# Performance work log

Hardware: AMD Instinct MI355X
Metric: run time of the kernel (lower is better)

The kernel has to match this reference:

```python
import jax, jax.numpy as jnp
import numpy as np

L, B, E, H, V, T = 512, 64, 256, 256, 32000, 50


def setup_inputs() -> dict:
    key = jax.random.key(0)
    ks = jax.random.split(key, 8)
    s_cell = 1.0 / np.sqrt(H + E)
    s_out = 1.0 / np.sqrt(2 * H)
    return {
        "text": jax.random.randint(ks[0], (L, B), 0, V, dtype=jnp.int64),
        "emb": jax.random.normal(ks[1], (V, E), dtype=jnp.float32),
        "W_f": jax.random.uniform(ks[2], (H, H + E), jnp.float32, -s_cell, s_cell),
        "b_f": jax.random.uniform(ks[3], (H,), jnp.float32, -s_cell, s_cell),
        "W_b": jax.random.uniform(ks[4], (H, H + E), jnp.float32, -s_cell, s_cell),
        "b_b": jax.random.uniform(ks[5], (H,), jnp.float32, -s_cell, s_cell),
        "W_out": jax.random.uniform(ks[6], (T, 2 * H), jnp.float32, -s_out, s_out),
        "b_out": jax.random.uniform(ks[7], (T,), jnp.float32, -s_out, s_out),
    }


def _rnn_scan(x_seq, W, b, batch, hidden):
    # x_seq: [L, B, E]; cell: h' = sigmoid(Linear(cat([x, h])))
    h0 = jnp.zeros((batch, hidden), dtype=x_seq.dtype)

    def step(h, x):
        h_new = jax.nn.sigmoid(jnp.concatenate([x, h], axis=1) @ W.T + b)
        return h_new, h_new

    _, hs = jax.lax.scan(step, h0, x_seq)
    return hs  # [L, B, H]


def reference(text, emb, W_f, b_f, W_b, b_b, W_out, b_out):
    # text: [L, B] int
    x = emb[text]  # [L, B, E]
    lr = _rnn_scan(x, W_f, b_f, x.shape[1], W_f.shape[0])  # [L, B, H]
    # backward cell processes reversed input; rl_tensor[i] = hidden after
    # processing positions L-1 .. L-1-i (NOT re-flipped, matching the source).
    rl = _rnn_scan(x[::-1], W_b, b_b, x.shape[1], W_b.shape[0])  # [L, B, H]
    hidden = jnp.concatenate([lr, rl], axis=2)  # [L, B, 2H]
    out = hidden @ W_out.T + b_out  # [L, B, T]
    return out, hidden
```

## Files before the change

kernel.cpp:

```cpp
#include <hip/hip_runtime.h>
#include <stdint.h>

#define L_SEQ 512
#define BATCH 64
#define KTOT  512
#define TDIM  50
#define HID2  512
#define ROWSTRIDE ((long)BATCH * HID2)
#define NLOG2E 1.4426950408889634f

typedef __attribute__((ext_vector_type(8))) short bf16x8;
typedef __attribute__((ext_vector_type(4))) float f32x4;

static __device__ __forceinline__ unsigned short f2bf(float f) {
  union { float f; unsigned int u; } v; v.f = f;
  unsigned int r = (v.u + 0x7FFFu + ((v.u >> 16) & 1u)) >> 16;
  return (unsigned short)r;
}

static __device__ __forceinline__ bf16x8 pack8(const float* f) {
  bf16x8 r;
#pragma unroll
  for (int i = 0; i < 8; ++i) r[i] = (short)f2bf(f[i]);
  return r;
}

static __device__ __forceinline__ unsigned cvt_pk_bf16(float a, float b) {
  unsigned r;
  asm("v_cvt_pk_bf16_f32 %0, %1, %2" : "=v"(r) : "v"(a), "v"(b));
  return r;
}

__global__ __launch_bounds__(512) void pre_kernel(
    const int* __restrict__ text, const float* __restrict__ emb,
    const float* __restrict__ W_f, const float* __restrict__ b_f,
    const float* __restrict__ W_b, const float* __restrict__ b_b,
    float* __restrict__ hidden) {
  const int blk = blockIdx.x;
  const int dir = blk >> 8;
  const int base = (blk & 255) * 128;
  const float* W    = dir ? W_b : W_f;
  const float* bias = dir ? b_b : b_f;
  const int tid = threadIdx.x;
  const int w = tid >> 6, ln = tid & 63, m16 = ln & 15, g4 = ln >> 4;

  __shared__ __align__(16) unsigned char xLds[16 * 512];

  bf16x8 wfrag[2][8];
#pragma unroll
  for (int t = 0; t < 2; ++t) {
    const int j0 = w * 32 + t * 16 + m16;
#pragma unroll
    for (int kk = 0; kk < 8; ++kk) {
      const float* p = W + (long)j0 * KTOT + kk * 32 + g4 * 8;
      float4 p0 = *(const float4*)(p);
      float4 p1 = *(const float4*)(p + 4);
      float f[8] = {p0.x, p0.y, p0.z, p0.w, p1.x, p1.y, p1.z, p1.w};
      wfrag[t][kk] = pack8(f);
    }
  }
  float biasr[2][4];
#pragma unroll
  for (int t = 0; t < 2; ++t)
#pragma unroll
    for (int r = 0; r < 4; ++r) biasr[t][r] = bias[w * 32 + t * 16 + 4 * g4 + r];

  const int xm = tid >> 5;
  const int e0 = (tid & 31) * 8;

  for (int mt = 0; mt < 8; ++mt) {
    const int g = base + mt * 16 + xm;
    const int l = g >> 6, b = g & 63;
    const int srcl = dir ? (L_SEQ - 1 - l) : l;
    const int tok = text[srcl * BATCH + b];
    const float* xp = emb + (long)tok * 256 + e0;
    float4 a0 = *(const float4*)(xp);
    float4 a1 = *(const float4*)(xp + 4);
    float f[8] = {a0.x, a0.y, a0.z, a0.w, a1.x, a1.y, a1.z, a1.w};
    bf16x8 xv = pack8(f);
    if (mt) __syncthreads();
    *(bf16x8*)(xLds + xm * 512 + ((e0 * 2) ^ ((xm & 7) << 4))) = xv;
    __syncthreads();

    f32x4 acc0 = {0.f, 0.f, 0.f, 0.f};
    f32x4 acc1 = {0.f, 0.f, 0.f, 0.f};
#pragma unroll
    for (int kk = 0; kk < 8; ++kk) {
      bf16x8 uf = *(const bf16x8*)(xLds + m16 * 512 +
                                   (((kk * 64) + g4 * 16) ^ ((m16 & 7) << 4)));
      acc0 = __builtin_amdgcn_mfma_f32_16x16x32_bf16(wfrag[0][kk], uf, acc0, 0, 0, 0);
      acc1 = __builtin_amdgcn_mfma_f32_16x16x32_bf16(wfrag[1][kk], uf, acc1, 0, 0, 0);
    }
    const int gg = base + mt * 16 + m16;
    float* op = hidden + (long)gg * HID2 + dir * 256 + w * 32 + 4 * g4;
    *(float4*)(op)      = make_float4(-NLOG2E * (acc0[0] + biasr[0][0]),
                                      -NLOG2E * (acc0[1] + biasr[0][1]),
                                      -NLOG2E * (acc0[2] + biasr[0][2]),
                                      -NLOG2E * (acc0[3] + biasr[0][3]));
    *(float4*)(op + 16) = make_float4(-NLOG2E * (acc1[0] + biasr[1][0]),
                                      -NLOG2E * (acc1[1] + biasr[1][1]),
                                      -NLOG2E * (acc1[2] + biasr[1][2]),
                                      -NLOG2E * (acc1[3] + biasr[1][3]));
  }
}

__global__ __launch_bounds__(512, 1) void scan_kernel(
    const float* __restrict__ W_f, const float* __restrict__ W_b,
    float* __restrict__ hidden) {
  const int wg  = blockIdx.x;
  const int dir = wg >> 2;
  const int b0  = (wg & 3) * 16;
  const int tid = threadIdx.x;
  const int w = tid >> 6, ln = tid & 63, m16 = ln & 15, g4 = ln >> 4;
  const float* W = dir ? W_b : W_f;

  __shared__ __align__(16) unsigned char hLds[2][8 * 1024];

  bf16x8 wfrag[2][8];
#pragma unroll
  for (int t = 0; t < 2; ++t) {
    const int j0 = w * 32 + t * 16 + m16;
#pragma unroll
    for (int kk = 0; kk < 8; ++kk) {
      const float* p = W + (long)j0 * KTOT + 256 + kk * 32 + g4 * 8;
      float4 p0 = *(const float4*)(p);
      float4 p1 = *(const float4*)(p + 4);
      float f[8] = {-NLOG2E * p0.x, -NLOG2E * p0.y, -NLOG2E * p0.z, -NLOG2E * p0.w,
                    -NLOG2E * p1.x, -NLOG2E * p1.y, -NLOG2E * p1.z, -NLOG2E * p1.w};
      wfrag[t][kk] = pack8(f);
    }
  }

  int rdoff[8];
#pragma unroll
  for (int kk = 0; kk < 8; ++kk) rdoff[kk] = kk * 1024 + ln * 16;
  const int wroff0 = w * 1024 + ((g4 >> 1) * 256) + m16 * 16 + (g4 & 1) * 8;
  const int wroff1 = wroff0 + 512;

  *(f32x4*)(&hLds[0][0] + tid * 16) = f32x4{0.f, 0.f, 0.f, 0.f};

  const long roff = (long)(b0 + m16) * HID2 + dir * 256 + w * 32 + 4 * g4;

  f32x4 pA0, pA1, pB0, pB1;
  pA0 = *(const f32x4*)(hidden + roff);
  pA1 = *(const f32x4*)(hidden + roff + 16);
  pB0 = *(const f32x4*)(hidden + ROWSTRIDE + roff);
  pB1 = *(const f32x4*)(hidden + ROWSTRIDE + roff + 16);

  __syncthreads();

#define STEP(BUF, PF0, PF1, SROW)                                              \
  {                                                                            \
    bf16x8 uf[8];                                                              \
    _Pragma("unroll")                                                          \
    for (int kk = 0; kk < 8; ++kk)                                             \
      uf[kk] = *(const bf16x8*)(&hLds[BUF][0] + rdoff[kk]);                    \
    f32x4 acc0 = {0.f, 0.f, 0.f, 0.f};                                         \
    f32x4 acc1 = {0.f, 0.f, 0.f, 0.f};                                         \
    _Pragma("unroll")                                                          \
    for (int kk = 0; kk < 8; ++kk) {                                           \
      acc0 = __builtin_amdgcn_mfma_f32_16x16x32_bf16(wfrag[0][kk], uf[kk],     \
                                                     acc0, 0, 0, 0);           \
      acc1 = __builtin_amdgcn_mfma_f32_16x16x32_bf16(wfrag[1][kk], uf[kk],     \
                                                     acc1, 0, 0, 0);           \
    }                                                                          \
    float h0[4], h1[4];                                                        \
    _Pragma("unroll")                                                          \
    for (int r = 0; r < 4; ++r) {                                              \
      h0[r] = __builtin_amdgcn_rcpf(                                           \
          1.f + __builtin_amdgcn_exp2f(acc0[r] + PF0[r]));                     \
      h1[r] = __builtin_amdgcn_rcpf(                                           \
          1.f + __builtin_amdgcn_exp2f(acc1[r] + PF1[r]));                     \
    }                                                                          \
    *(uint2*)(&hLds[(BUF) ^ 1][0] + wroff0) =                                  \
        make_uint2(cvt_pk_bf16(h0[0], h0[1]), cvt_pk_bf16(h0[2], h0[3]));      \
    *(uint2*)(&hLds[(BUF) ^ 1][0] + wroff1) =                                  \
        make_uint2(cvt_pk_bf16(h1[0], h1[1]), cvt_pk_bf16(h1[2], h1[3]));      \
    float* gp = hidden + (long)(SROW)*ROWSTRIDE + roff;                        \
    *(float4*)(gp)      = make_float4(h0[0], h0[1], h0[2], h0[3]);             \
    *(float4*)(gp + 16) = make_float4(h1[0], h1[1], h1[2], h1[3]);             \
    {                                                                          \
      const long rn = ((SROW) + 2 < L_SEQ) ? (SROW) + 2 : L_SEQ - 1;           \
      const float* lp = hidden + rn * ROWSTRIDE + roff;                        \
      PF0 = *(const f32x4*)(lp);                                               \
      PF1 = *(const f32x4*)(lp + 16);                                          \
    }                                                                          \
    asm volatile("s_waitcnt lgkmcnt(0)" ::: "memory");                         \
    __builtin_amdgcn_s_barrier();                                              \
    asm volatile("" ::: "memory");                                             \
  }

  for (int s = 0; s < L_SEQ; s += 2) {
    STEP(0, pA0, pA1, s)
    STEP(1, pB0, pB1, s + 1)
  }
#undef STEP
}

__global__ __launch_bounds__(64) void out_kernel(
    const float* __restrict__ hidden, const float* __restrict__ W_out,
    const float* __restrict__ b_out, float* __restrict__ out) {
  const int m0 = blockIdx.x * 16;
  const int ln = threadIdx.x;
  const int m16 = ln & 15, g4 = ln >> 4;

  bf16x8 a[16];
  const float* hp = hidden + (long)(m0 + m16) * HID2 + g4 * 8;
#pragma unroll
  for (int kk = 0; kk < 16; ++kk) {
    float4 p0 = *(const float4*)(hp + kk * 32);
    float4 p1 = *(const float4*)(hp + kk * 32 + 4);
    float f[8] = {p0.x, p0.y, p0.z, p0.w, p1.x, p1.y, p1.z, p1.w};
    a[kk] = pack8(f);
  }
#pragma unroll
  for (int nt = 0; nt < 4; ++nt) {
    const int trow = nt * 16 + m16;
    const bool valid = trow < TDIM;
    f32x4 acc = {0.f, 0.f, 0.f, 0.f};
    const float* wp = W_out + (long)trow * HID2 + g4 * 8;
#pragma unroll
    for (int kk = 0; kk < 16; ++kk) {
      bf16x8 bf;
      if (valid) {
        float4 p0 = *(const float4*)(wp + kk * 32);
        float4 p1 = *(const float4*)(wp + kk * 32 + 4);
        float f[8] = {p0.x, p0.y, p0.z, p0.w, p1.x, p1.y, p1.z, p1.w};
        bf = pack8(f);
      } else {
#pragma unroll
        for (int i = 0; i < 8; ++i) bf[i] = 0;
      }
      acc = __builtin_amdgcn_mfma_f32_16x16x32_bf16(a[kk], bf, acc, 0, 0, 0);
    }
    if (valid) {
      float bo = b_out[trow];
#pragma unroll
      for (int r = 0; r < 4; ++r)
        out[(long)(m0 + 4 * g4 + r) * TDIM + trow] = acc[r] + bo;
    }
  }
}

extern "C" void kernel_launch(void* const* d_in, const int* in_sizes, int n_in,
                              void* d_out, int out_size, void* d_ws, size_t ws_size,
                              hipStream_t stream) {
  const int*   text  = (const int*)d_in[0];
  const float* emb   = (const float*)d_in[1];
  const float* W_f   = (const float*)d_in[2];
  const float* b_f   = (const float*)d_in[3];
  const float* W_b   = (const float*)d_in[4];
  const float* b_b   = (const float*)d_in[5];
  const float* W_out = (const float*)d_in[6];
  const float* b_out = (const float*)d_in[7];
  float* out    = (float*)d_out;
  float* hidden = out + (long)L_SEQ * BATCH * TDIM;

  pre_kernel<<<512, 512, 0, stream>>>(text, emb, W_f, b_f, W_b, b_b, hidden);
  scan_kernel<<<8, 512, 0, stream>>>(W_f, W_b, hidden);
  out_kernel<<<2048, 64, 0, stream>>>(hidden, W_out, b_out, out);
}
```

Before: 446.0 us.

## Retile output projection kernel to reuse W_out fragments across two M tiles

The output projection kernel now runs 256-thread blocks where each wave computes two 16-row M tiles, so every converted W_out fragment feeds two MFMAs instead of one. Conversion to bf16 switches to the packed hardware convert instruction. Out-of-range T rows now load row 0 unconditionally instead of branching, which removes divergence. The grid shrinks from 2048 to 256 blocks, which lowers parallelism and raises register pressure. The output kernel is likely a small part of total time next to the serial scan.

Measured after the change: 430.3 us. -3.5%, faster.

```diff
diff --git a/kernel.cpp b/kernel.cpp
--- a/kernel.cpp
+++ b/kernel.cpp
@@ -29,6 +29,15 @@
   unsigned r;
   asm("v_cvt_pk_bf16_f32 %0, %1, %2" : "=v"(r) : "v"(a), "v"(b));
   return r;
+}
+
+static __device__ __forceinline__ bf16x8 pack8f(const float* f) {
+  union { bf16x8 v; unsigned u[4]; } o;
+  o.u[0] = cvt_pk_bf16(f[0], f[1]);
+  o.u[1] = cvt_pk_bf16(f[2], f[3]);
+  o.u[2] = cvt_pk_bf16(f[4], f[5]);
+  o.u[3] = cvt_pk_bf16(f[6], f[7]);
+  return o.v;
 }
 
 __global__ __launch_bounds__(512) void pre_kernel(
@@ -197,47 +206,55 @@
 #undef STEP
 }
 
-__global__ __launch_bounds__(64) void out_kernel(
+__global__ __launch_bounds__(256, 1) void out_kernel(
     const float* __restrict__ hidden, const float* __restrict__ W_out,
     const float* __restrict__ b_out, float* __restrict__ out) {
-  const int m0 = blockIdx.x * 16;
-  const int ln = threadIdx.x;
-  const int m16 = ln & 15, g4 = ln >> 4;
-
-  bf16x8 a[16];
-  const float* hp = hidden + (long)(m0 + m16) * HID2 + g4 * 8;
-#pragma unroll
-  for (int kk = 0; kk < 16; ++kk) {
-    float4 p0 = *(const float4*)(hp + kk * 32);
-    float4 p1 = *(const float4*)(hp + kk * 32 + 4);
-    float f[8] = {p0.x, p0.y, p0.z, p0.w, p1.x, p1.y, p1.z, p1.w};
-    a[kk] = pack8(f);
-  }
+  const int tid = threadIdx.x;
+  const int w = tid >> 6, ln = tid & 63, m16 = ln & 15, g4 = ln >> 4;
+  const int mtA = (blockIdx.x * 4 + w) * 2;
+  const int mtB = mtA + 1;
+
+  bf16x8 aA[16], aB[16];
+  {
+    const float* hpA = hidden + (long)(mtA * 16 + m16) * HID2 + g4 * 8;
+    const float* hpB = hidden + (long)(mtB * 16 + m16) * HID2 + g4 * 8;
+#pragma unroll
+    for (int kk = 0; kk < 16; ++kk) {
+      float4 p0 = *(const float4*)(hpA + kk * 32);
+      float4 p1 = *(const float4*)(hpA + kk * 32 + 4);
+      float f[8] = {p0.x, p0.y, p0.z, p0.w, p1.x, p1.y, p1.z, p1.w};
+      aA[kk] = pack8f(f);
+      float4 q0 = *(const float4*)(hpB + kk * 32);
+      float4 q1 = *(const float4*)(hpB + kk * 32 + 4);
+      float g[8] = {q0.x, q0.y, q0.z, q0.w, q1.x, q1.y, q1.z, q1.w};
+      aB[kk] = pack8f(g);
+    }
+  }
+
 #pragma unroll
   for (int nt = 0; nt < 4; ++nt) {
     const int trow = nt * 16 + m16;
+    const int rrow = trow < TDIM ? trow : 0;
     const bool valid = trow < TDIM;
-    f32x4 acc = {0.f, 0.f, 0.f, 0.f};
-    const float* wp = W_out + (long)trow * HID2 + g4 * 8;
+    f32x4 accA = {0.f, 0.f, 0.f, 0.f};
+    f32x4 accB = {0.f, 0.f, 0.f, 0.f};
+    const float* wp = W_out + (long)rrow * HID2 + g4 * 8;
 #pragma unroll
     for (int kk = 0; kk < 16; ++kk) {
-      bf16x8 bf;
-      if (valid) {
-        float4 p0 = *(const float4*)(wp + kk * 32);
-        float4 p1 = *(const float4*)(wp + kk * 32 + 4);
-        float f[8] = {p0.x, p0.y, p0.z, p0.w, p1.x, p1.y, p1.z, p1.w};
-        bf = pack8(f);
-      } else {
-#pragma unroll
-        for (int i = 0; i < 8; ++i) bf[i] = 0;
+      float4 p0 = *(const float4*)(wp + kk * 32);
+      float4 p1 = *(const float4*)(wp + kk * 32 + 4);
+      float f[8] = {p0.x, p0.y, p0.z, p0.w, p1.x, p1.y, p1.z, p1.w};
+      bf16x8 bf = pack8f(f);
+      accA = __builtin_amdgcn_mfma_f32_16x16x32_bf16(aA[kk], bf, accA, 0, 0, 0);
+      accB = __builtin_amdgcn_mfma_f32_16x16x32_bf16(aB[kk], bf, accB, 0, 0, 0);
+    }
+    if (valid) {
+      const float bo = b_out[trow];
+#pragma unroll
+      for (int r = 0; r < 4; ++r) {
+        out[(long)(mtA * 16 + 4 * g4 + r) * TDIM + trow] = accA[r] + bo;
+        out[(long)(mtB * 16 + 4 * g4 + r) * TDIM + trow] = accB[r] + bo;
       }
-      acc = __builtin_amdgcn_mfma_f32_16x16x32_bf16(a[kk], bf, acc, 0, 0, 0);
-    }
-    if (valid) {
-      float bo = b_out[trow];
-#pragma unroll
-      for (int r = 0; r < 4; ++r)
-        out[(long)(m0 + 4 * g4 + r) * TDIM + trow] = acc[r] + bo;
     }
   }
 }
@@ -258,5 +275,5 @@
 
   pre_kernel<<<512, 512, 0, stream>>>(text, emb, W_f, b_f, W_b, b_b, hidden);
   scan_kernel<<<8, 512, 0, stream>>>(W_f, W_b, hidden);
-  out_kernel<<<2048, 64, 0, stream>>>(hidden, W_out, b_out, out);
-}
+  out_kernel<<<256, 256, 0, stream>>>(hidden, W_out, b_out, out);
+}
```
